# Optimization experiments

Measured on AMD Instinct MI355X. Metric: run time of the kernel, lower is better.

## Reference

```python
import jax, jax.numpy as jnp
import numpy as np

B, N, DIM = 8, 4096, 128

def setup_inputs() -> dict:
    key = jax.random.key(0)
    ks = jax.random.split(key, 6)
    s = 1.0 / np.sqrt(DIM)
    return {
        "x": jax.random.normal(ks[0], (B, N, DIM), dtype=jnp.float32),
        "q_global": jax.random.normal(ks[1], (B, N, DIM), dtype=jnp.float32),
        "Wkv": jax.random.normal(ks[2], (DIM, 2 * DIM), dtype=jnp.float32) * s,
        "bkv": jax.random.normal(ks[3], (2 * DIM,), dtype=jnp.float32) * 0.02,
        "Wp": jax.random.normal(ks[4], (DIM, DIM), dtype=jnp.float32) * s,
        "bp": jax.random.normal(ks[5], (DIM,), dtype=jnp.float32) * 0.02,
    }

def reference(x, q_global, Wkv, bkv, Wp, bp):
    # x: [B, n, dim]; kv linear -> split into k, v (each [B, n, dim])
    kv = x @ Wkv + bkv
    k, v = jnp.split(kv, 2, axis=-1)
    dim = x.shape[-1]
    q = q_global * (1.0 / jnp.sqrt(jnp.asarray(dim, x.dtype)))
    # scores = k @ q^T : [B, n, m]; softmax over query axis m (as in source)
    scores = jnp.einsum("bnd,bmd->bnm", k, q)
    attn = jax.nn.softmax(scores, axis=-1)
    # attention @ v : contracts m against v's row index (m == n)
    out = jnp.einsum("bnm,bmd->bnd", attn, v)
    return out @ Wp + bp
```

## Files before the change

### kernel.cpp

```cpp
#include <hip/hip_runtime.h>

typedef __bf16 bf16x8 __attribute__((ext_vector_type(8)));
typedef float f32x4 __attribute__((ext_vector_type(4)));
typedef float f32x16 __attribute__((ext_vector_type(16)));

struct alignas(16) US8 { unsigned short us[8]; };

static __device__ inline unsigned short f2bf(float f) {
  union { float f; unsigned u; } v; v.f = f;
  unsigned r = v.u + 0x7fffu + ((v.u >> 16) & 1u);
  return (unsigned short)(r >> 16);
}

static __device__ inline void gload16(const unsigned short* g, unsigned short* l) {
  __builtin_amdgcn_global_load_lds(
      (const __attribute__((address_space(1))) void*)g,
      (__attribute__((address_space(3))) void*)l, 16, 0, 0);
}

#define NSEQ 4096
#define DIM 128
#define ROWS 32768
#define KH 2

#define EXPC (1.4426950408889634f * 0.08838834764831845f)

__global__ void prep_kernel(const float* __restrict__ Wkv, const float* __restrict__ Wp,
                            unsigned short* __restrict__ wkvT, unsigned short* __restrict__ wpT) {
  const int t = threadIdx.x;
  const int d = (t & 63) * 2;
  if (blockIdx.x < 64) {
    const int col = blockIdx.x * 4 + (t >> 6);
    unsigned short lo = f2bf(Wkv[d * 256 + col]);
    unsigned short hi = f2bf(Wkv[(d + 1) * 256 + col]);
    *reinterpret_cast<unsigned*>(&wkvT[col * 128 + d]) = (unsigned)lo | ((unsigned)hi << 16);
  } else {
    const int col = (blockIdx.x - 64) * 4 + (t >> 6);
    unsigned short lo = f2bf(Wp[d * 128 + col]);
    unsigned short hi = f2bf(Wp[(d + 1) * 128 + col]);
    *reinterpret_cast<unsigned*>(&wpT[col * 128 + d]) = (unsigned)lo | ((unsigned)hi << 16);
  }
}

__global__ __launch_bounds__(256, 2) void kv_kernel(
    const float* __restrict__ x, const unsigned short* __restrict__ wkvT,
    const float* __restrict__ bkv, const float* __restrict__ q,
    unsigned short* __restrict__ kout, unsigned short* __restrict__ vtout,
    unsigned short* __restrict__ qo) {
  const int tid = threadIdx.x;
  if (blockIdx.x >= 256) {
    int i = ((blockIdx.x - 256) * 256 + tid) * 8;
    const float4* p = reinterpret_cast<const float4*>(q + i);
    float4 a = p[0], b = p[1];
    US8 o;
    o.us[0]=f2bf(a.x*EXPC); o.us[1]=f2bf(a.y*EXPC); o.us[2]=f2bf(a.z*EXPC); o.us[3]=f2bf(a.w*EXPC);
    o.us[4]=f2bf(b.x*EXPC); o.us[5]=f2bf(b.y*EXPC); o.us[6]=f2bf(b.z*EXPC); o.us[7]=f2bf(b.w*EXPC);
    int row = i >> 7, d0 = i & 127;
    int bb = row >> 12, n = row & (NSEQ - 1), tile = n >> 6, l = n & 63, kc = d0 >> 3;
    *reinterpret_cast<US8*>(qo + (size_t)bb * NSEQ * DIM + tile * 8192 + kc * 512 + l * 8) = o;
    return;
  }
  __shared__ __align__(16) unsigned short WT[256 * 136];
  const int wv = tid >> 6, lane = tid & 63, l16 = lane & 15, quad = lane >> 4;
  const int row0 = blockIdx.x * 128;

  for (int p = 0; p < 16; ++p) {
    int c = p * 256 + tid;
    int col = c >> 4, c16 = c & 15;
    *reinterpret_cast<US8*>(&WT[col * 136 + c16 * 8]) =
        *reinterpret_cast<const US8*>(wkvT + col * 128 + c16 * 8);
  }
  __syncthreads();

  bf16x8 afrag[2][4];
  for (int rg = 0; rg < 2; ++rg) {
    const int arow = row0 + wv * 32 + rg * 16 + l16;
    for (int s = 0; s < 4; ++s) {
      const float4* xp = reinterpret_cast<const float4*>(x + (size_t)arow * DIM + s * 32 + quad * 8);
      float4 u0 = xp[0], u1 = xp[1];
      US8 af;
      af.us[0]=f2bf(u0.x); af.us[1]=f2bf(u0.y); af.us[2]=f2bf(u0.z); af.us[3]=f2bf(u0.w);
      af.us[4]=f2bf(u1.x); af.us[5]=f2bf(u1.y); af.us[6]=f2bf(u1.z); af.us[7]=f2bf(u1.w);
      afrag[rg][s] = __builtin_bit_cast(bf16x8, af);
    }
  }
  f32x4 acc[2][16];
  for (int rg = 0; rg < 2; ++rg)
    for (int g = 0; g < 16; ++g) acc[rg][g] = f32x4{0.f, 0.f, 0.f, 0.f};
  for (int s = 0; s < 4; ++s)
    for (int g = 0; g < 16; ++g) {
      bf16x8 bfr = *reinterpret_cast<const bf16x8*>(&WT[(g * 16 + l16) * 136 + s * 32 + quad * 8]);
      acc[0][g] = __builtin_amdgcn_mfma_f32_16x16x32_bf16(afrag[0][s], bfr, acc[0][g], 0, 0, 0);
      acc[1][g] = __builtin_amdgcn_mfma_f32_16x16x32_bf16(afrag[1][s], bfr, acc[1][g], 0, 0, 0);
    }

  for (int rg = 0; rg < 2; ++rg)
    for (int g = 0; g < 8; ++g) {
      float bias = bkv[g * 16 + l16];
      for (int r = 0; r < 4; ++r) {
        int orow = row0 + wv * 32 + rg * 16 + quad * 4 + r;
        kout[(size_t)orow * DIM + g * 16 + l16] = f2bf(acc[rg][g][r] + bias);
      }
    }
  __syncthreads();
  unsigned short* LDSt = WT;
  for (int rg = 0; rg < 2; ++rg)
    for (int g = 0; g < 8; ++g) {
      float bias = bkv[128 + g * 16 + l16];
      for (int r = 0; r < 4; ++r)
        LDSt[(g * 16 + l16) * 140 + wv * 32 + rg * 16 + quad * 4 + r] = f2bf(acc[rg][g + 8][r] + bias);
    }
  __syncthreads();
  const int bb = row0 >> 12, tilebase = (row0 & (NSEQ - 1)) >> 6;
  unsigned short* vbo = vtout + (size_t)bb * NSEQ * DIM;
  for (int p = 0; p < 8; ++p) {
    int c = p * 256 + tid;
    int tl = c >> 10, u = c & 1023, idx = u >> 6, l = u & 63;
    int mg = idx >> 1, dh = idx & 1, d = dh * 64 + l;
    int nb = tl * 64 + (mg >> 1) * 16 + (mg & 1) * 4;
    uint2 lo = *reinterpret_cast<const uint2*>(&LDSt[d * 140 + nb]);
    uint2 hi = *reinterpret_cast<const uint2*>(&LDSt[d * 140 + nb + 8]);
    uint4 o{lo.x, lo.y, hi.x, hi.y};
    *reinterpret_cast<uint4*>(vbo + (size_t)(tilebase + tl) * 8192 + idx * 512 + l * 8) = o;
  }
}

__global__ __launch_bounds__(256, 2) void attn_kernel(
    const unsigned short* __restrict__ kbuf, const unsigned short* __restrict__ qblk,
    const unsigned short* __restrict__ vblk,
    float* __restrict__ opart, float* __restrict__ lpart) {
  __shared__ __align__(16) unsigned short SH[16384];
  unsigned short* Ksh = SH;
  unsigned short* Vsh = SH + 8192;
  const int tid = threadIdx.x;
  const int wv = tid >> 6, lane = tid & 63, l32 = lane & 31, h = lane >> 5;
  const int b = blockIdx.x & 7;
  const int t = blockIdx.x >> 3;
  const int q0 = (t & 31) * 128;
  const int kh = t >> 5;
  const int key0 = kh * (NSEQ / KH);
  const unsigned short* kb = kbuf + (size_t)b * NSEQ * DIM;
  const unsigned short* qb = qblk + (size_t)b * NSEQ * DIM;
  const unsigned short* vb = vblk + (size_t)b * NSEQ * DIM;

  bf16x8 kfrag[8];
  for (int ks = 0; ks < 8; ++ks)
    kfrag[ks] = __builtin_bit_cast(bf16x8, *reinterpret_cast<const US8*>(
        kb + (size_t)(q0 + wv * 32 + l32) * DIM + ks * 16 + h * 8));

  f32x16 Oacc[4];
  for (int dt = 0; dt < 4; ++dt)
    for (int i = 0; i < 16; ++i) Oacc[dt][i] = 0.f;
  float lsum = 0.f;

  for (int it = 0; it < NSEQ / KH / 64; ++it) {
    const int tile = (key0 + it * 64) >> 6;
    __syncthreads();
    for (int c = 0; c < 8; ++c) {
      int idx = wv * 8 + c;
      if (idx < 16)
        gload16(qb + (size_t)tile * 8192 + idx * 512 + lane * 8, &Ksh[idx * 512]);
      else
        gload16(vb + (size_t)tile * 8192 + (idx - 16) * 512 + lane * 8, &Vsh[(idx - 16) * 512]);
    }
    __syncthreads();

    f32x16 S0, S1;
    for (int i = 0; i < 16; ++i) { S0[i] = 0.f; S1[i] = 0.f; }
    for (int ks = 0; ks < 8; ++ks) {
      const unsigned short* kc = &Ksh[(ks * 2 + h) * 512];
      bf16x8 a0 = *reinterpret_cast<const bf16x8*>(&kc[l32 * 8]);
      bf16x8 a1 = *reinterpret_cast<const bf16x8*>(&kc[(32 + l32) * 8]);
      S0 = __builtin_amdgcn_mfma_f32_32x32x16_bf16(a0, kfrag[ks], S0, 0, 0, 0);
      S1 = __builtin_amdgcn_mfma_f32_32x32x16_bf16(a1, kfrag[ks], S1, 0, 0, 0);
    }

    bf16x8 pf[2][2];
    for (int T = 0; T < 2; ++T) {
      unsigned pk[8];
      for (int i2 = 0; i2 < 8; ++i2) {
        float e0 = exp2f(T ? S1[i2 * 2] : S0[i2 * 2]);
        float e1 = exp2f(T ? S1[i2 * 2 + 1] : S0[i2 * 2 + 1]);
        unsigned u0 = __builtin_bit_cast(unsigned, e0) & 0xffff0000u;
        unsigned u1 = __builtin_bit_cast(unsigned, e1) & 0xffff0000u;
        lsum += __builtin_bit_cast(float, u0) + __builtin_bit_cast(float, u1);
        pk[i2] = (u0 >> 16) | u1;
      }
      pf[T][0] = __builtin_bit_cast(bf16x8, uint4{pk[0], pk[1], pk[2], pk[3]});
      pf[T][1] = __builtin_bit_cast(bf16x8, uint4{pk[4], pk[5], pk[6], pk[7]});
    }

    for (int T = 0; T < 2; ++T)
      for (int s = 0; s < 2; ++s) {
        const int mg = 4 * T + 2 * s + h;
        for (int dt = 0; dt < 4; ++dt) {
          bf16x8 bv = *reinterpret_cast<const bf16x8*>(
              &Vsh[(mg * 2 + (dt >> 1)) * 512 + ((dt & 1) * 32 + l32) * 8]);
          Oacc[dt] = __builtin_amdgcn_mfma_f32_32x32x16_bf16(pf[T][s], bv, Oacc[dt], 0, 0, 0);
        }
      }
  }

  {
    float v = lsum;
    v += __shfl_xor(v, 32);
    if (lane < 32)
      lpart[(size_t)kh * ROWS + (size_t)b * NSEQ + q0 + wv * 32 + l32] = v;
  }
  float* ob = opart + (size_t)kh * ROWS * DIM + ((size_t)b * NSEQ + q0 + wv * 32) * DIM;
  for (int dt = 0; dt < 4; ++dt)
    for (int i = 0; i < 16; ++i) {
      int n = (i & 3) + 8 * (i >> 2) + 4 * h;
      ob[n * DIM + dt * 32 + l32] = Oacc[dt][i];
    }
}

__global__ __launch_bounds__(256, 2) void combine_proj_kernel(
    const float* __restrict__ opart, const float* __restrict__ lpart,
    const unsigned short* __restrict__ wpT, const float* __restrict__ bp,
    float* __restrict__ out) {
  __shared__ __align__(16) unsigned short WT[128 * 136];
  const int tid = threadIdx.x;
  const int wv = tid >> 6, lane = tid & 63, l16 = lane & 15, quad = lane >> 4;
  const int row0 = blockIdx.x * 128;

  for (int p = 0; p < 8; ++p) {
    int c = p * 256 + tid;
    int col = c >> 4, c16 = c & 15;
    *reinterpret_cast<US8*>(&WT[col * 136 + c16 * 8]) =
        *reinterpret_cast<const US8*>(wpT + col * 128 + c16 * 8);
  }
  __syncthreads();

  f32x4 acc[2][8];
  for (int rg = 0; rg < 2; ++rg)
    for (int g = 0; g < 8; ++g) acc[rg][g] = f32x4{0.f, 0.f, 0.f, 0.f};
  for (int rg = 0; rg < 2; ++rg) {
    const int arow = row0 + wv * 32 + rg * 16 + l16;
    float linv = 1.f / (lpart[arow] + lpart[ROWS + arow]);
    for (int s = 0; s < 4; ++s) {
      const size_t base = (size_t)arow * DIM + s * 32 + quad * 8;
      float4 s0 = *reinterpret_cast<const float4*>(opart + base);
      float4 s1 = *reinterpret_cast<const float4*>(opart + base + 4);
      float4 u0 = *reinterpret_cast<const float4*>(opart + (size_t)ROWS * DIM + base);
      float4 u1 = *reinterpret_cast<const float4*>(opart + (size_t)ROWS * DIM + base + 4);
      US8 af;
      af.us[0]=f2bf((s0.x+u0.x)*linv); af.us[1]=f2bf((s0.y+u0.y)*linv);
      af.us[2]=f2bf((s0.z+u0.z)*linv); af.us[3]=f2bf((s0.w+u0.w)*linv);
      af.us[4]=f2bf((s1.x+u1.x)*linv); af.us[5]=f2bf((s1.y+u1.y)*linv);
      af.us[6]=f2bf((s1.z+u1.z)*linv); af.us[7]=f2bf((s1.w+u1.w)*linv);
      bf16x8 a = __builtin_bit_cast(bf16x8, af);
      for (int g = 0; g < 8; ++g) {
        bf16x8 bfr = *reinterpret_cast<const bf16x8*>(&WT[(g * 16 + l16) * 136 + s * 32 + quad * 8]);
        acc[rg][g] = __builtin_amdgcn_mfma_f32_16x16x32_bf16(a, bfr, acc[rg][g], 0, 0, 0);
      }
    }
  }
  for (int rg = 0; rg < 2; ++rg)
    for (int g = 0; g < 8; ++g) {
      float bias = bp[g * 16 + l16];
      for (int r = 0; r < 4; ++r) {
        int orow = row0 + wv * 32 + rg * 16 + quad * 4 + r;
        out[(size_t)orow * DIM + g * 16 + l16] = acc[rg][g][r] + bias;
      }
    }
}

extern "C" void kernel_launch(void* const* d_in, const int* in_sizes, int n_in,
                              void* d_out, int out_size, void* d_ws, size_t ws_size,
                              hipStream_t stream) {
  (void)in_sizes; (void)n_in; (void)out_size; (void)ws_size;
  const float* x   = (const float*)d_in[0];
  const float* qg  = (const float*)d_in[1];
  const float* Wkv = (const float*)d_in[2];
  const float* bkv = (const float*)d_in[3];
  const float* Wp  = (const float*)d_in[4];
  const float* bp  = (const float*)d_in[5];
  float* out = (float*)d_out;

  unsigned short* qbf  = (unsigned short*)d_ws;
  unsigned short* kbf  = qbf + (size_t)ROWS * DIM;
  unsigned short* vtbf = kbf + (size_t)ROWS * DIM;
  unsigned short* wkvT = vtbf + (size_t)ROWS * DIM;
  unsigned short* wpT  = wkvT + 256 * 128;
  float* lpart = (float*)(wpT + 128 * 128);
  float* opart = lpart + (size_t)KH * ROWS;

  hipLaunchKernelGGL(prep_kernel, dim3(96), dim3(256), 0, stream, Wkv, Wp, wkvT, wpT);
  hipLaunchKernelGGL(kv_kernel, dim3(256 + 2048), dim3(256), 0, stream,
                     x, wkvT, bkv, qg, kbf, vtbf, qbf);
  hipLaunchKernelGGL(attn_kernel, dim3(8 * 32 * KH), dim3(256), 0, stream, kbf, qbf, vtbf, opart, lpart);
  hipLaunchKernelGGL(combine_proj_kernel, dim3(ROWS / 128), dim3(256), 0, stream, opart, lpart, wpT, bp, out);
}
```

Measured before the change: 189.4 us.

## Double-buffer attention K/V tile loads and halve rows per block in GEMM kernels

```diff
diff --git a/kernel.cpp b/kernel.cpp
--- a/kernel.cpp
+++ b/kernel.cpp
@@ -48,8 +48,8 @@
     unsigned short* __restrict__ kout, unsigned short* __restrict__ vtout,
     unsigned short* __restrict__ qo) {
   const int tid = threadIdx.x;
-  if (blockIdx.x >= 256) {
-    int i = ((blockIdx.x - 256) * 256 + tid) * 8;
+  if (blockIdx.x >= 512) {
+    int i = ((blockIdx.x - 512) * 256 + tid) * 8;
     const float4* p = reinterpret_cast<const float4*>(q + i);
     float4 a = p[0], b = p[1];
     US8 o;
@@ -62,7 +62,7 @@
   }
   __shared__ __align__(16) unsigned short WT[256 * 136];
   const int wv = tid >> 6, lane = tid & 63, l16 = lane & 15, quad = lane >> 4;
-  const int row0 = blockIdx.x * 128;
+  const int row0 = blockIdx.x * 64;
 
   for (int p = 0; p < 16; ++p) {
     int c = p * 256 + tid;
@@ -72,56 +72,51 @@
   }
   __syncthreads();
 
-  bf16x8 afrag[2][4];
-  for (int rg = 0; rg < 2; ++rg) {
-    const int arow = row0 + wv * 32 + rg * 16 + l16;
-    for (int s = 0; s < 4; ++s) {
-      const float4* xp = reinterpret_cast<const float4*>(x + (size_t)arow * DIM + s * 32 + quad * 8);
-      float4 u0 = xp[0], u1 = xp[1];
-      US8 af;
-      af.us[0]=f2bf(u0.x); af.us[1]=f2bf(u0.y); af.us[2]=f2bf(u0.z); af.us[3]=f2bf(u0.w);
-      af.us[4]=f2bf(u1.x); af.us[5]=f2bf(u1.y); af.us[6]=f2bf(u1.z); af.us[7]=f2bf(u1.w);
-      afrag[rg][s] = __builtin_bit_cast(bf16x8, af);
-    }
-  }
-  f32x4 acc[2][16];
-  for (int rg = 0; rg < 2; ++rg)
-    for (int g = 0; g < 16; ++g) acc[rg][g] = f32x4{0.f, 0.f, 0.f, 0.f};
+  bf16x8 afrag[4];
+  const int arow = row0 + wv * 16 + l16;
+  for (int s = 0; s < 4; ++s) {
+    const float4* xp = reinterpret_cast<const float4*>(x + (size_t)arow * DIM + s * 32 + quad * 8);
+    float4 u0 = xp[0], u1 = xp[1];
+    US8 af;
+    af.us[0]=f2bf(u0.x); af.us[1]=f2bf(u0.y); af.us[2]=f2bf(u0.z); af.us[3]=f2bf(u0.w);
+    af.us[4]=f2bf(u1.x); af.us[5]=f2bf(u1.y); af.us[6]=f2bf(u1.z); af.us[7]=f2bf(u1.w);
+    afrag[s] = __builtin_bit_cast(bf16x8, af);
+  }
+  f32x4 acc[16];
+  for (int g = 0; g < 16; ++g) acc[g] = f32x4{0.f, 0.f, 0.f, 0.f};
   for (int s = 0; s < 4; ++s)
     for (int g = 0; g < 16; ++g) {
       bf16x8 bfr = *reinterpret_cast<const bf16x8*>(&WT[(g * 16 + l16) * 136 + s * 32 + quad * 8]);
-      acc[0][g] = __builtin_amdgcn_mfma_f32_16x16x32_bf16(afrag[0][s], bfr, acc[0][g], 0, 0, 0);
-      acc[1][g] = __builtin_amdgcn_mfma_f32_16x16x32_bf16(afrag[1][s], bfr, acc[1][g], 0, 0, 0);
-    }
-
-  for (int rg = 0; rg < 2; ++rg)
-    for (int g = 0; g < 8; ++g) {
-      float bias = bkv[g * 16 + l16];
-      for (int r = 0; r < 4; ++r) {
-        int orow = row0 + wv * 32 + rg * 16 + quad * 4 + r;
-        kout[(size_t)orow * DIM + g * 16 + l16] = f2bf(acc[rg][g][r] + bias);
-      }
-    }
+      acc[g] = __builtin_amdgcn_mfma_f32_16x16x32_bf16(afrag[s], bfr, acc[g], 0, 0, 0);
+    }
+
+  for (int g = 0; g < 8; ++g) {
+    float bias = bkv[g * 16 + l16];
+    for (int r = 0; r < 4; ++r) {
+      int orow = row0 + wv * 16 + quad * 4 + r;
+      kout[(size_t)orow * DIM + g * 16 + l16] = f2bf(acc[g][r] + bias);
+    }
+  }
   __syncthreads();
   unsigned short* LDSt = WT;
-  for (int rg = 0; rg < 2; ++rg)
-    for (int g = 0; g < 8; ++g) {
-      float bias = bkv[128 + g * 16 + l16];
-      for (int r = 0; r < 4; ++r)
-        LDSt[(g * 16 + l16) * 140 + wv * 32 + rg * 16 + quad * 4 + r] = f2bf(acc[rg][g + 8][r] + bias);
-    }
-  __syncthreads();
-  const int bb = row0 >> 12, tilebase = (row0 & (NSEQ - 1)) >> 6;
-  unsigned short* vbo = vtout + (size_t)bb * NSEQ * DIM;
-  for (int p = 0; p < 8; ++p) {
+  for (int g = 0; g < 8; ++g) {
+    float bias = bkv[128 + g * 16 + l16];
+    for (int r = 0; r < 4; ++r)
+      LDSt[(g * 16 + l16) * 72 + wv * 16 + quad * 4 + r] = f2bf(acc[g + 8][r] + bias);
+  }
+  __syncthreads();
+  const int bb = row0 >> 12;
+  const int tile = (row0 & (NSEQ - 1)) >> 6;
+  unsigned short* vbo = vtout + (size_t)bb * NSEQ * DIM + (size_t)tile * 8192;
+  for (int p = 0; p < 4; ++p) {
     int c = p * 256 + tid;
-    int tl = c >> 10, u = c & 1023, idx = u >> 6, l = u & 63;
+    int idx = c >> 6, l = c & 63;
     int mg = idx >> 1, dh = idx & 1, d = dh * 64 + l;
-    int nb = tl * 64 + (mg >> 1) * 16 + (mg & 1) * 4;
-    uint2 lo = *reinterpret_cast<const uint2*>(&LDSt[d * 140 + nb]);
-    uint2 hi = *reinterpret_cast<const uint2*>(&LDSt[d * 140 + nb + 8]);
+    int nb = (mg >> 1) * 16 + (mg & 1) * 4;
+    uint2 lo = *reinterpret_cast<const uint2*>(&LDSt[d * 72 + nb]);
+    uint2 hi = *reinterpret_cast<const uint2*>(&LDSt[d * 72 + nb + 8]);
     uint4 o{lo.x, lo.y, hi.x, hi.y};
-    *reinterpret_cast<uint4*>(vbo + (size_t)(tilebase + tl) * 8192 + idx * 512 + l * 8) = o;
+    *reinterpret_cast<uint4*>(vbo + (size_t)idx * 512 + l * 8) = o;
   }
 }
 
@@ -129,9 +124,7 @@
     const unsigned short* __restrict__ kbuf, const unsigned short* __restrict__ qblk,
     const unsigned short* __restrict__ vblk,
     float* __restrict__ opart, float* __restrict__ lpart) {
-  __shared__ __align__(16) unsigned short SH[16384];
-  unsigned short* Ksh = SH;
-  unsigned short* Vsh = SH + 8192;
+  __shared__ __align__(16) unsigned short SH[32768];
   const int tid = threadIdx.x;
   const int wv = tid >> 6, lane = tid & 63, l32 = lane & 31, h = lane >> 5;
   const int b = blockIdx.x & 7;
@@ -143,6 +136,20 @@
   const unsigned short* qb = qblk + (size_t)b * NSEQ * DIM;
   const unsigned short* vb = vblk + (size_t)b * NSEQ * DIM;
 
+  const unsigned short* gsrc[8];
+  int lofs[8];
+#pragma unroll
+  for (int c = 0; c < 8; ++c) {
+    const int idx = wv * 8 + c;
+    const unsigned short* p = (idx < 16) ? (qb + idx * 512) : (vb + (size_t)(idx - 16) * 512);
+    gsrc[c] = p + (size_t)(key0 >> 6) * 8192 + lane * 8;
+    lofs[c] = idx * 512;
+  }
+
+  constexpr int NT = NSEQ / KH / 64;
+#pragma unroll
+  for (int c = 0; c < 8; ++c) gload16(gsrc[c], &SH[lofs[c]]);
+
   bf16x8 kfrag[8];
   for (int ks = 0; ks < 8; ++ks)
     kfrag[ks] = __builtin_bit_cast(bf16x8, *reinterpret_cast<const US8*>(
@@ -153,17 +160,18 @@
     for (int i = 0; i < 16; ++i) Oacc[dt][i] = 0.f;
   float lsum = 0.f;
 
-  for (int it = 0; it < NSEQ / KH / 64; ++it) {
-    const int tile = (key0 + it * 64) >> 6;
-    __syncthreads();
-    for (int c = 0; c < 8; ++c) {
-      int idx = wv * 8 + c;
-      if (idx < 16)
-        gload16(qb + (size_t)tile * 8192 + idx * 512 + lane * 8, &Ksh[idx * 512]);
-      else
-        gload16(vb + (size_t)tile * 8192 + (idx - 16) * 512 + lane * 8, &Vsh[(idx - 16) * 512]);
-    }
-    __syncthreads();
+  __syncthreads();
+
+  for (int it = 0; it < NT; ++it) {
+    const int cur = (it & 1) << 14;
+    if (it + 1 < NT) {
+      const int nxt = cur ^ 16384;
+#pragma unroll
+      for (int c = 0; c < 8; ++c)
+        gload16(gsrc[c] + (size_t)(it + 1) * 8192, &SH[nxt + lofs[c]]);
+    }
+    const unsigned short* Ksh = SH + cur;
+    const unsigned short* Vsh = Ksh + 8192;
 
     f32x16 S0, S1;
     for (int i = 0; i < 16; ++i) { S0[i] = 0.f; S1[i] = 0.f; }
@@ -199,6 +207,8 @@
           Oacc[dt] = __builtin_amdgcn_mfma_f32_32x32x16_bf16(pf[T][s], bv, Oacc[dt], 0, 0, 0);
         }
       }
+
+    __syncthreads();
   }
 
   {
@@ -222,7 +232,7 @@
   __shared__ __align__(16) unsigned short WT[128 * 136];
   const int tid = threadIdx.x;
   const int wv = tid >> 6, lane = tid & 63, l16 = lane & 15, quad = lane >> 4;
-  const int row0 = blockIdx.x * 128;
+  const int row0 = blockIdx.x * 64;
 
   for (int p = 0; p < 8; ++p) {
     int c = p * 256 + tid;
@@ -232,38 +242,34 @@
   }
   __syncthreads();
 
-  f32x4 acc[2][8];
-  for (int rg = 0; rg < 2; ++rg)
-    for (int g = 0; g < 8; ++g) acc[rg][g] = f32x4{0.f, 0.f, 0.f, 0.f};
-  for (int rg = 0; rg < 2; ++rg) {
-    const int arow = row0 + wv * 32 + rg * 16 + l16;
-    float linv = 1.f / (lpart[arow] + lpart[ROWS + arow]);
-    for (int s = 0; s < 4; ++s) {
-      const size_t base = (size_t)arow * DIM + s * 32 + quad * 8;
-      float4 s0 = *reinterpret_cast<const float4*>(opart + base);
-      float4 s1 = *reinterpret_cast<const float4*>(opart + base + 4);
-      float4 u0 = *reinterpret_cast<const float4*>(opart + (size_t)ROWS * DIM + base);
-      float4 u1 = *reinterpret_cast<const float4*>(opart + (size_t)ROWS * DIM + base + 4);
-      US8 af;
-      af.us[0]=f2bf((s0.x+u0.x)*linv); af.us[1]=f2bf((s0.y+u0.y)*linv);
-      af.us[2]=f2bf((s0.z+u0.z)*linv); af.us[3]=f2bf((s0.w+u0.w)*linv);
-      af.us[4]=f2bf((s1.x+u1.x)*linv); af.us[5]=f2bf((s1.y+u1.y)*linv);
-      af.us[6]=f2bf((s1.z+u1.z)*linv); af.us[7]=f2bf((s1.w+u1.w)*linv);
-      bf16x8 a = __builtin_bit_cast(bf16x8, af);
-      for (int g = 0; g < 8; ++g) {
-        bf16x8 bfr = *reinterpret_cast<const bf16x8*>(&WT[(g * 16 + l16) * 136 + s * 32 + quad * 8]);
-        acc[rg][g] = __builtin_amdgcn_mfma_f32_16x16x32_bf16(a, bfr, acc[rg][g], 0, 0, 0);
-      }
-    }
-  }
-  for (int rg = 0; rg < 2; ++rg)
+  f32x4 acc[8];
+  for (int g = 0; g < 8; ++g) acc[g] = f32x4{0.f, 0.f, 0.f, 0.f};
+  const int arow = row0 + wv * 16 + l16;
+  float linv = 1.f / (lpart[arow] + lpart[ROWS + arow]);
+  for (int s = 0; s < 4; ++s) {
+    const size_t base = (size_t)arow * DIM + s * 32 + quad * 8;
+    float4 s0 = *reinterpret_cast<const float4*>(opart + base);
+    float4 s1 = *reinterpret_cast<const float4*>(opart + base + 4);
+    float4 u0 = *reinterpret_cast<const float4*>(opart + (size_t)ROWS * DIM + base);
+    float4 u1 = *reinterpret_cast<const float4*>(opart + (size_t)ROWS * DIM + base + 4);
+    US8 af;
+    af.us[0]=f2bf((s0.x+u0.x)*linv); af.us[1]=f2bf((s0.y+u0.y)*linv);
+    af.us[2]=f2bf((s0.z+u0.z)*linv); af.us[3]=f2bf((s0.w+u0.w)*linv);
+    af.us[4]=f2bf((s1.x+u1.x)*linv); af.us[5]=f2bf((s1.y+u1.y)*linv);
+    af.us[6]=f2bf((s1.z+u1.z)*linv); af.us[7]=f2bf((s1.w+u1.w)*linv);
+    bf16x8 a = __builtin_bit_cast(bf16x8, af);
     for (int g = 0; g < 8; ++g) {
-      float bias = bp[g * 16 + l16];
-      for (int r = 0; r < 4; ++r) {
-        int orow = row0 + wv * 32 + rg * 16 + quad * 4 + r;
-        out[(size_t)orow * DIM + g * 16 + l16] = acc[rg][g][r] + bias;
-      }
-    }
+      bf16x8 bfr = *reinterpret_cast<const bf16x8*>(&WT[(g * 16 + l16) * 136 + s * 32 + quad * 8]);
+      acc[g] = __builtin_amdgcn_mfma_f32_16x16x32_bf16(a, bfr, acc[g], 0, 0, 0);
+    }
+  }
+  for (int g = 0; g < 8; ++g) {
+    float bias = bp[g * 16 + l16];
+    for (int r = 0; r < 4; ++r) {
+      int orow = row0 + wv * 16 + quad * 4 + r;
+      out[(size_t)orow * DIM + g * 16 + l16] = acc[g][r] + bias;
+    }
+  }
 }
 
 extern "C" void kernel_launch(void* const* d_in, const int* in_sizes, int n_in,
@@ -287,8 +293,8 @@
   float* opart = lpart + (size_t)KH * ROWS;
 
   hipLaunchKernelGGL(prep_kernel, dim3(96), dim3(256), 0, stream, Wkv, Wp, wkvT, wpT);
-  hipLaunchKernelGGL(kv_kernel, dim3(256 + 2048), dim3(256), 0, stream,
+  hipLaunchKernelGGL(kv_kernel, dim3(512 + 2048), dim3(256), 0, stream,
                      x, wkvT, bkv, qg, kbf, vtbf, qbf);
   hipLaunchKernelGGL(attn_kernel, dim3(8 * 32 * KH), dim3(256), 0, stream, kbf, qbf, vtbf, opart, lpart);
-  hipLaunchKernelGGL(combine_proj_kernel, dim3(ROWS / 128), dim3(256), 0, stream, opart, lpart, wpT, bp, out);
-}
+  hipLaunchKernelGGL(combine_proj_kernel, dim3(ROWS / 64), dim3(256), 0, stream, opart, lpart, wpT, bp, out);
+}
```

New measurement: 185.5 us. 1.02x faster.
